# Kernel optimization log

Hardware: AMD Instinct MI355X
Metric: run time of the kernel (lower is better)

The kernel has to match this reference:

```python
import jax, jax.numpy as jnp
import numpy as np

NUM_HEADS = 16


def _window_for_epoch(epoch: int) -> int:
    # Faithful reproduction of the module's (buggy) branch structure:
    # epoch<5 sets mask_4, elif epoch<10 sets mask_6, but then an
    # independent `if epoch < 15` overwrites with mask_8, else mask_10.
    if epoch < 15:
        return 16  # mask_8 -> w=16
    return 20      # mask_10 -> w=20


def setup_inputs() -> dict:
    key = jax.random.key(0)
    ks = jax.random.split(key, 4)
    B, N, C = 2, 2048, 1024
    x = jax.random.normal(ks[0], (B, N, C), dtype=jnp.float32)
    qkv_w = jax.random.normal(ks[1], (3 * C, C), dtype=jnp.float32) * (C ** -0.5)
    proj_w = jax.random.normal(ks[2], (C, C), dtype=jnp.float32) * (C ** -0.5)
    proj_b = jnp.zeros((C,), dtype=jnp.float32)
    return {"x": x, "qkv_w": qkv_w, "proj_w": proj_w, "proj_b": proj_b, "epoch": 0}


def reference(x, qkv_w, proj_w, proj_b, epoch):
    B, N, C = x.shape
    H = NUM_HEADS
    Dh = C // H
    scale = float(Dh // H)  # head_dim // num_heads (integer division), =4

    qkv = jnp.einsum('bnc,dc->bnd', x, qkv_w)           # [B,N,3C]
    qkv = qkv.reshape(B, N, 3, H, Dh).transpose(2, 0, 3, 1, 4)
    q, k, v = qkv[0], qkv[1], qkv[2]                    # each [B,H,N,Dh]

    attn = jnp.einsum('bhnd,bhmd->bhnm', q, k) * scale  # [B,H,N,N]

    w = _window_for_epoch(int(epoch))
    idx = jnp.arange(N)
    band = jnp.abs(idx[:, None] - idx[None, :]) <= w    # [N,N] sliding window
    # Original fills masked logits with 1e-9 (NOT -inf) before softmax.
    attn = jnp.where(band[None, None], attn, jnp.float32(1e-9))
    attn = jax.nn.softmax(attn, axis=-1)

    out = jnp.einsum('bhnm,bhmd->bhnd', attn, v)        # [B,H,N,Dh]
    out = out.transpose(0, 2, 1, 3).reshape(B, N, C)
    out = jnp.einsum('bnc,dc->bnd', out, proj_w) + proj_b
    return out
```

## Files before the change

kernel.cpp:

```cpp
#include <hip/hip_runtime.h>
#include <cstddef>


typedef _Float16 f16x8 __attribute__((ext_vector_type(8)));
typedef float    f32x4 __attribute__((ext_vector_type(4)));

#define MFMA16(a, b, c) __builtin_amdgcn_mfma_f32_16x16x32_f16((a), (b), (c), 0, 0, 0)

__device__ __forceinline__ void gl_lds16(const void* g, void* l) {
    __builtin_amdgcn_global_load_lds(
        (const __attribute__((address_space(1))) void*)g,
        (__attribute__((address_space(3))) void*)l, 16, 0, 0);
}

__device__ __forceinline__ ushort f2h(float f) {
    _Float16 h = (_Float16)f;
    return *(ushort*)&h;
}

__global__ void split_all(const float* __restrict__ x,
                          const float* __restrict__ qkvw,
                          const float* __restrict__ projw,
                          ushort* __restrict__ x16,
                          ushort* __restrict__ w16,
                          ushort* __restrict__ pw16,
                          float* __restrict__ sall)
{
    const int i = blockIdx.x * 256 + threadIdx.x;
    if (i < 512) ((float4*)sall)[i] = make_float4(0.f, 0.f, 0.f, 0.f);
    const float* src; ushort* dst; int j;
    if (i < 1048576)      { src = x;     dst = x16;  j = i; }
    else if (i < 1835008) { src = qkvw;  dst = w16;  j = i - 1048576; }
    else                  { src = projw; dst = pw16; j = i - 1835008; }

    float4 v = ((const float4*)src)[j];
    ((ushort4*)dst)[j] = make_ushort4(f2h(v.x), f2h(v.y), f2h(v.z), f2h(v.w));
}

__global__ __launch_bounds__(256, 3) void gemm_mfma(
    const ushort* __restrict__ A_g, const ushort* __restrict__ W_g,
    ushort* __restrict__ out16, float* __restrict__ sall, int K)
{
    __shared__ ushort smem[16384];
    ushort* AS0 = smem;
    ushort* AS1 = smem + 4096;
    ushort* WS0 = smem + 8192;
    ushort* WS1 = smem + 12288;

    const int tid  = threadIdx.x;
    const int wid  = tid >> 6;
    const int lane = tid & 63;
    const int quad = lane >> 4;
    const int cl   = lane & 15;
    const int m0 = blockIdx.y * 128;
    const int n0 = blockIdx.x * 128;
    const int wm = (wid & 1) * 64;
    const int wn = (wid >> 1) * 64;

    const int srow = lane >> 2;
    const int scol = (lane & 3) * 8;

    const ushort* src = (wid < 2) ? A_g : W_g;
    ushort* dst = smem + wid * 4096;
    const int r0 = (wid < 2) ? m0 : n0;
    const int cofs = (wid & 1) * 32;

    f32x4 acc[4][4];
#pragma unroll
    for (int i = 0; i < 4; ++i)
#pragma unroll
        for (int j = 0; j < 4; ++j) acc[i][j] = (f32x4){0.f, 0.f, 0.f, 0.f};

    for (int k0 = 0; k0 < K; k0 += 64) {
#pragma unroll
        for (int c = 0; c < 8; ++c)
            gl_lds16(src + (size_t)(r0 + c * 16 + srow) * K + k0 + cofs + scol,
                     dst + c * 512);
        __syncthreads();

        f16x8 a0[4], w0[4];
#pragma unroll
        for (int i = 0; i < 4; ++i) {
            a0[i] = ((const f16x8*)AS0)[(wm + i * 16 + cl) * 4 + quad];
            w0[i] = ((const f16x8*)WS0)[(wn + i * 16 + cl) * 4 + quad];
        }
#pragma unroll
        for (int mi = 0; mi < 4; ++mi)
#pragma unroll
            for (int ni = 0; ni < 4; ++ni)
                acc[mi][ni] = MFMA16(a0[mi], w0[ni], acc[mi][ni]);

        f16x8 a1[4], w1[4];
#pragma unroll
        for (int i = 0; i < 4; ++i) {
            a1[i] = ((const f16x8*)AS1)[(wm + i * 16 + cl) * 4 + quad];
            w1[i] = ((const f16x8*)WS1)[(wn + i * 16 + cl) * 4 + quad];
        }
#pragma unroll
        for (int mi = 0; mi < 4; ++mi)
#pragma unroll
            for (int ni = 0; ni < 4; ++ni)
                acc[mi][ni] = MFMA16(a1[mi], w1[ni], acc[mi][ni]);
        __syncthreads();
    }

#pragma unroll
    for (int mi = 0; mi < 4; ++mi)
#pragma unroll
        for (int r = 0; r < 4; ++r) {
            const int gm = m0 + wm + mi * 16 + quad * 4 + r;
            const int b  = gm >> 11;
            const int nn = gm & 2047;
#pragma unroll
            for (int ni = 0; ni < 4; ++ni) {
                const int gn = n0 + wn + ni * 16 + cl;
                const int s  = gn >> 10;
                const int h  = (gn >> 6) & 15;
                const int dh = gn & 63;
                out16[(size_t)s * 4194304u + (((size_t)b * 16 + h) * 2048 + nn) * 64 + dh]
                    = f2h(acc[mi][ni][r]);
            }
        }

    if (n0 >= 2048) {
        const int b = (m0 + wm) >> 11;
        const int h = ((n0 + wn) >> 6) & 15;
#pragma unroll
        for (int ni = 0; ni < 4; ++ni) {
            float ps = 0.f;
#pragma unroll
            for (int mi = 0; mi < 4; ++mi)
#pragma unroll
                for (int r = 0; r < 4; ++r) ps += acc[mi][ni][r];
            ps += __shfl_xor(ps, 16);
            ps += __shfl_xor(ps, 32);
            if (quad == 0)
                atomicAdd(&sall[(b * 16 + h) * 64 + ni * 16 + cl], ps);
        }
    }
}

__global__ __launch_bounds__(256, 2) void gemm_proj(
    const ushort* __restrict__ A_g, const ushort* __restrict__ W_g,
    const float* __restrict__ bias, float* __restrict__ out)
{
    const int K = 1024, Nout = 1024;
    __shared__ ushort smem[24576];

    const int tid  = threadIdx.x;
    const int wid  = tid >> 6;
    const int lane = tid & 63;
    const int quad = lane >> 4;
    const int cl   = lane & 15;
    const int m0 = blockIdx.y * 64;
    const int n0 = blockIdx.x * 128;
    const int wm = (wid & 1) * 32;
    const int wn = (wid >> 1) * 64;

    const int srow = lane >> 2;
    const int scol = (lane & 3) * 8;

    f32x4 acc[2][4];
#pragma unroll
    for (int i = 0; i < 2; ++i)
#pragma unroll
        for (int j = 0; j < 4; ++j) acc[i][j] = (f32x4){0.f, 0.f, 0.f, 0.f};

    for (int k0 = 0; k0 < K; k0 += 128) {
#pragma unroll
        for (int c = 0; c < 12; ++c) {
            const int cid = wid * 12 + c;
            const ushort* s; ushort* d; int rr, pl;
            if (cid < 16) {
                pl = cid >> 2;
                const int ch = cid & 3;
                s = A_g; rr = m0 + ch * 16;
                d = smem + pl * 2048 + ch * 512;
            } else {
                const int wc = cid - 16;
                pl = wc >> 3;
                const int ch = wc & 7;
                s = W_g; rr = n0 + ch * 16;
                d = smem + 8192 + pl * 4096 + ch * 512;
            }
            gl_lds16(s + (size_t)(rr + srow) * K + k0 + pl * 32 + scol, d);
        }
        __syncthreads();

#pragma unroll
        for (int pl = 0; pl < 4; ++pl) {
            const ushort* ASp = smem + pl * 2048;
            const ushort* WSp = smem + 8192 + pl * 4096;
            f16x8 a[2], w[4];
#pragma unroll
            for (int i = 0; i < 2; ++i)
                a[i] = ((const f16x8*)ASp)[(wm + i * 16 + cl) * 4 + quad];
#pragma unroll
            for (int i = 0; i < 4; ++i)
                w[i] = ((const f16x8*)WSp)[(wn + i * 16 + cl) * 4 + quad];
#pragma unroll
            for (int mi = 0; mi < 2; ++mi)
#pragma unroll
                for (int ni = 0; ni < 4; ++ni)
                    acc[mi][ni] = MFMA16(a[mi], w[ni], acc[mi][ni]);
        }
        __syncthreads();
    }

    float bb[4];
#pragma unroll
    for (int ni = 0; ni < 4; ++ni) bb[ni] = bias[n0 + wn + ni * 16 + cl];
#pragma unroll
    for (int mi = 0; mi < 2; ++mi)
#pragma unroll
        for (int r = 0; r < 4; ++r) {
            const int gm = m0 + wm + mi * 16 + quad * 4 + r;
            float* rowp = out + (size_t)gm * Nout;
#pragma unroll
            for (int ni = 0; ni < 4; ++ni) {
                const int gn = n0 + wn + ni * 16 + cl;
                rowp[gn] = acc[mi][ni][r] + bb[ni];
            }
        }
}

__global__ __launch_bounds__(512) void attn_mfma(
    const ushort* __restrict__ qg, const ushort* __restrict__ kg,
    const ushort* __restrict__ vg,
    const float* __restrict__ sall,
    ushort* __restrict__ outp,
    const int* __restrict__ epoch_ptr)
{
    const int N = 2048;
    const int w = (epoch_ptr[0] < 15) ? 16 : 20;

    __shared__ ushort Pl[8][16][72];
    __shared__ ushort VT[64][180];

    const int tid  = threadIdx.x;
    const int wid  = tid >> 6;
    const int lane = tid & 63;
    const int quad = lane >> 4;
    const int cl   = lane & 15;

    const int bh = blockIdx.x >> 4;
    const int n0 = (blockIdx.x & 15) << 7;
    const int lo = max(0, n0 - w);
    const int wm = wid << 4;
    const int hi = min(N - 1, n0 + 127 + w);
    const int cnt = hi - lo + 1;

    for (int t = tid; t < 64 * 26; t += 512) {
        const int row = t / 26;
        const int c2  = 128 + (t - row * 26) * 2;
        *(unsigned*)&VT[row][c2] = 0u;
    }
    __syncthreads();

    for (int t = tid; t < 168 * 8; t += 512) {
        const int s  = t >> 3;
        const int db = (t & 7) * 8;
        if (s < cnt) {
            uint4 vv = *(const uint4*)(vg + (((size_t)bh * N) + lo + s) * 64 + db);
            VT[db + 0][s] = (ushort)(vv.x & 0xffff); VT[db + 1][s] = (ushort)(vv.x >> 16);
            VT[db + 2][s] = (ushort)(vv.y & 0xffff); VT[db + 3][s] = (ushort)(vv.y >> 16);
            VT[db + 4][s] = (ushort)(vv.z & 0xffff); VT[db + 5][s] = (ushort)(vv.z >> 16);
            VT[db + 6][s] = (ushort)(vv.w & 0xffff); VT[db + 7][s] = (ushort)(vv.w >> 16);
        }
    }

    const int jminw = max(0, n0 + wm - w);
    const int sbase = ((jminw - lo) >> 3) << 3;

    const ushort* qp = qg + ((size_t)bh * N + n0 + wm + cl) * 64;
    const f16x8 aq0 = *(const f16x8*)(qp + quad * 8);
    const f16x8 aq1 = *(const f16x8*)(qp + 32 + quad * 8);

    f32x4 sacc[4];
#pragma unroll
    for (int ni = 0; ni < 4; ++ni) {
        int krow = lo + sbase + ni * 16 + cl;
        krow = min(krow, N - 1);
        const ushort* kp = kg + ((size_t)bh * N + krow) * 64;
        const f16x8 bk0 = *(const f16x8*)(kp + quad * 8);
        const f16x8 bk1 = *(const f16x8*)(kp + 32 + quad * 8);
        f32x4 s = (f32x4){0.f, 0.f, 0.f, 0.f};
        s = MFMA16(aq0, bk0, s);
        s = MFMA16(aq1, bk1, s);
        sacc[ni] = s;
    }
#pragma unroll
    for (int ni = 0; ni < 4; ++ni) sacc[ni] *= 4.0f;

    float pm[4];
#pragma unroll
    for (int r = 0; r < 4; ++r) {
        const int n = n0 + wm + quad * 4 + r;
        const int jlo = max(0, n - w), jhi = min(N - 1, n + w);
        const int bc = jhi - jlo + 1;
        float mx = 1e-9f;
#pragma unroll
        for (int ni = 0; ni < 4; ++ni) {
            const int j = lo + sbase + ni * 16 + cl;
            const bool val = (j >= n - w) && (j <= n + w) && (j < N);
            const float sv = sacc[ni][r];
            if (val) mx = fmaxf(mx, sv);
        }
        mx = fmaxf(mx, __shfl_xor(mx, 1));
        mx = fmaxf(mx, __shfl_xor(mx, 2));
        mx = fmaxf(mx, __shfl_xor(mx, 4));
        mx = fmaxf(mx, __shfl_xor(mx, 8));
        const float em = __expf(1e-9f - mx);
        float e[4];
        float sum = 0.f;
#pragma unroll
        for (int ni = 0; ni < 4; ++ni) {
            const int j = lo + sbase + ni * 16 + cl;
            const bool val = (j >= n - w) && (j <= n + w) && (j < N);
            const float ev = val ? __expf(sacc[ni][r] - mx) : 0.f;
            e[ni] = val ? (ev - em) : 0.f;
            sum += ev;
        }
        sum += __shfl_xor(sum, 1);
        sum += __shfl_xor(sum, 2);
        sum += __shfl_xor(sum, 4);
        sum += __shfl_xor(sum, 8);
        const float inv = __builtin_amdgcn_rcpf((float)(N - bc) * em + sum);
        pm[r] = em * inv;
#pragma unroll
        for (int ni = 0; ni < 4; ++ni)
            sacc[ni][r] = e[ni] * inv;
    }

#pragma unroll
    for (int ni = 0; ni < 4; ++ni)
#pragma unroll
        for (int r = 0; r < 4; ++r)
            Pl[wid][quad * 4 + r][ni * 16 + cl] = f2h(sacc[ni][r]);

    __syncthreads();

    const int b = bh >> 4, h = bh & 15;
#pragma unroll
    for (int dn = 0; dn < 4; ++dn) {
        f32x4 o = (f32x4){0.f, 0.f, 0.f, 0.f};
#pragma unroll
        for (int k0 = 0; k0 < 64; k0 += 32) {
            const f16x8 a  = *(const f16x8*)&Pl[wid][cl][k0 + quad * 8];
            const f16x8 bb = *(const f16x8*)&VT[dn * 16 + cl][sbase + k0 + quad * 8];
            o = MFMA16(a, bb, o);
        }
        const int d = dn * 16 + cl;
        const float sv = sall[bh * 64 + d];
#pragma unroll
        for (int r = 0; r < 4; ++r) {
            const int n = n0 + wm + quad * 4 + r;
            outp[((size_t)b * N + n) * 1024 + h * 64 + d] = f2h(o[r] + pm[r] * sv);
        }
    }
}

extern "C" void kernel_launch(void* const* d_in, const int* in_sizes, int n_in,
                              void* d_out, int out_size, void* d_ws, size_t ws_size,
                              hipStream_t stream)
{
    const float* x      = (const float*)d_in[0];
    const float* qkv_w  = (const float*)d_in[1];
    const float* proj_w = (const float*)d_in[2];
    const float* proj_b = (const float*)d_in[3];
    const int*   epoch  = (const int*)d_in[4];
    float* out = (float*)d_out;

    const size_t BHND = (size_t)2 * 16 * 2048 * 64;
    const size_t XN = 4194304, WN = 3145728;

    ushort* qkv16 = (ushort*)d_ws;
    ushort* q16   = qkv16;
    ushort* k16   = qkv16 + BHND;
    ushort* v16   = qkv16 + 2 * BHND;
    float*  sall  = (float*)(qkv16 + 3 * BHND);
    ushort* x16   = (ushort*)(sall + 4096);
    ushort* w16   = x16 + XN;
    ushort* pw16  = w16 + WN;
    ushort* ao    = x16;

    split_all<<<dim3(8192), dim3(256), 0, stream>>>(
        x, qkv_w, proj_w, x16, w16, pw16, sall);

    gemm_mfma<<<dim3(24, 32), dim3(256), 0, stream>>>(x16, w16, qkv16, sall, 1024);

    attn_mfma<<<dim3(512), dim3(512), 0, stream>>>(q16, k16, v16, sall, ao, epoch);

    gemm_proj<<<dim3(8, 64), dim3(256), 0, stream>>>(ao, pw16, proj_b, out);
}
```

Before: 148.1 us.

## Rewrite QKV GEMM with 5-stage async LDS pipeline and larger swizzled tiles

Replaces the QKV projection GEMM with a 512-thread kernel using 256x192 tiles, a five-buffer global-to-LDS prefetch ring with partial vmcnt waits, XOR-swizzled LDS layout, block-index remapping for L2 locality, and raised MFMA priority. It is meant to hide global load latency behind MFMA work, cut LDS bank conflicts and improve data reuse compared with the single-stage 128x128 kernel that synchronised twice per K step. The trade-off is heavy LDS use (about 144 KB per block) and a 96-register accumulator per thread, which lowers occupancy, plus a grid of exactly 256 blocks.

New measurement: 145.3 us. About the same (-1.9%).

```diff
diff --git a/kernel.cpp b/kernel.cpp
--- a/kernel.cpp
+++ b/kernel.cpp
@@ -37,105 +37,148 @@
     ((ushort4*)dst)[j] = make_ushort4(f2h(v.x), f2h(v.y), f2h(v.z), f2h(v.w));
 }
 
-__global__ __launch_bounds__(256, 3) void gemm_mfma(
+__global__ __launch_bounds__(512, 2) void gemm_qkv_pipe(
     const ushort* __restrict__ A_g, const ushort* __restrict__ W_g,
-    ushort* __restrict__ out16, float* __restrict__ sall, int K)
+    ushort* __restrict__ out16, float* __restrict__ sall)
 {
-    __shared__ ushort smem[16384];
-    ushort* AS0 = smem;
-    ushort* AS1 = smem + 4096;
-    ushort* WS0 = smem + 8192;
-    ushort* WS1 = smem + 12288;
+    const int K = 1024;
+    __shared__ ushort sm[73728];
 
     const int tid  = threadIdx.x;
     const int wid  = tid >> 6;
     const int lane = tid & 63;
     const int quad = lane >> 4;
     const int cl   = lane & 15;
-    const int m0 = blockIdx.y * 128;
-    const int n0 = blockIdx.x * 128;
-    const int wm = (wid & 1) * 64;
-    const int wn = (wid >> 1) * 64;
-
-    const int srow = lane >> 2;
-    const int scol = (lane & 3) * 8;
-
-    const ushort* src = (wid < 2) ? A_g : W_g;
-    ushort* dst = smem + wid * 4096;
-    const int r0 = (wid < 2) ? m0 : n0;
-    const int cofs = (wid & 1) * 32;
-
-    f32x4 acc[4][4];
-#pragma unroll
-    for (int i = 0; i < 4; ++i)
-#pragma unroll
-        for (int j = 0; j < 4; ++j) acc[i][j] = (f32x4){0.f, 0.f, 0.f, 0.f};
-
-    for (int k0 = 0; k0 < K; k0 += 64) {
-#pragma unroll
-        for (int c = 0; c < 8; ++c)
-            gl_lds16(src + (size_t)(r0 + c * 16 + srow) * K + k0 + cofs + scol,
-                     dst + c * 512);
-        __syncthreads();
-
-        f16x8 a0[4], w0[4];
-#pragma unroll
-        for (int i = 0; i < 4; ++i) {
-            a0[i] = ((const f16x8*)AS0)[(wm + i * 16 + cl) * 4 + quad];
-            w0[i] = ((const f16x8*)WS0)[(wn + i * 16 + cl) * 4 + quad];
-        }
-#pragma unroll
-        for (int mi = 0; mi < 4; ++mi)
-#pragma unroll
-            for (int ni = 0; ni < 4; ++ni)
-                acc[mi][ni] = MFMA16(a0[mi], w0[ni], acc[mi][ni]);
-
-        f16x8 a1[4], w1[4];
-#pragma unroll
-        for (int i = 0; i < 4; ++i) {
-            a1[i] = ((const f16x8*)AS1)[(wm + i * 16 + cl) * 4 + quad];
-            w1[i] = ((const f16x8*)WS1)[(wn + i * 16 + cl) * 4 + quad];
-        }
-#pragma unroll
-        for (int mi = 0; mi < 4; ++mi)
-#pragma unroll
-            for (int ni = 0; ni < 4; ++ni)
-                acc[mi][ni] = MFMA16(a1[mi], w1[ni], acc[mi][ni]);
-        __syncthreads();
-    }
-
-#pragma unroll
-    for (int mi = 0; mi < 4; ++mi)
+
+    const int bsw = (blockIdx.x & 7) * 32 + (blockIdx.x >> 3);
+    const int m0 = (bsw >> 4) * 256;
+    const int n0 = (bsw & 15) * 192;
+
+    const int wr = wid >> 2;
+    const int wc = wid & 3;
+
+    const int lrow = lane >> 2;
+    const int sl   = lane & 3;
+    const int rA1 = wid * 16 + lrow;
+    const int rA2 = 128 + rA1;
+    const int rB1 = wid * 16 + lrow;
+    const int rB2 = 128 + (wid & 3) * 16 + lrow;
+
+    const ushort* sA1 = A_g + (size_t)(m0 + rA1) * K + ((sl ^ ((rA1 >> 1) & 3)) * 8);
+    const ushort* sA2 = A_g + (size_t)(m0 + rA2) * K + ((sl ^ ((rA2 >> 1) & 3)) * 8);
+    const ushort* sB1 = W_g + (size_t)(n0 + rB1) * K + ((sl ^ ((rB1 >> 1) & 3)) * 8);
+    const ushort* sB2 = W_g + (size_t)(n0 + rB2) * K + ((sl ^ ((rB2 >> 1) & 3)) * 8);
+
+    const int dA1 = wid * 512;
+    const int dA2 = 4096 + wid * 512;
+    const int dB1 = 8192 + wid * 512;
+
+    int aoff[8], boff[3];
+#pragma unroll
+    for (int mg = 0; mg < 8; ++mg) {
+        const int row = wr * 128 + mg * 16 + cl;
+        aoff[mg] = row * 32 + ((quad ^ ((row >> 1) & 3)) * 8);
+    }
+#pragma unroll
+    for (int ng = 0; ng < 3; ++ng) {
+        const int row = wc * 48 + ng * 16 + cl;
+        boff[ng] = 8192 + row * 32 + ((quad ^ ((row >> 1) & 3)) * 8);
+    }
+
+    f32x4 acc[8][3];
+#pragma unroll
+    for (int mg = 0; mg < 8; ++mg)
+#pragma unroll
+        for (int ng = 0; ng < 3; ++ng) acc[mg][ng] = (f32x4){0.f, 0.f, 0.f, 0.f};
+
+    int kst = 0;
+
+#define STAGE_T(BUF) do {                                                    \
+    const int bo_ = (BUF) * 14336;                                           \
+    gl_lds16(sA1 + kst, sm + bo_ + dA1);                                     \
+    gl_lds16(sA2 + kst, sm + bo_ + dA2);                                     \
+    gl_lds16(sB1 + kst, sm + bo_ + dB1);                                     \
+    ushort* pB2_ = (wid < 4) ? (sm + bo_ + 12288 + wid * 512)                \
+                             : (sm + 71680 + (wid & 3) * 512);               \
+    gl_lds16(sB2 + kst, pB2_);                                               \
+    kst += 32;                                                               \
+} while (0)
+
+#define COMPUTE_T(BUF) do {                                                  \
+    const int co_ = (BUF) * 14336;                                           \
+    f16x8 af[8]; f16x8 bf[3];                                                \
+    _Pragma("unroll")                                                        \
+    for (int mg = 0; mg < 8; ++mg) af[mg] = *(const f16x8*)&sm[co_ + aoff[mg]]; \
+    _Pragma("unroll")                                                        \
+    for (int ng = 0; ng < 3; ++ng) bf[ng] = *(const f16x8*)&sm[co_ + boff[ng]]; \
+    __builtin_amdgcn_s_setprio(1);                                           \
+    _Pragma("unroll")                                                        \
+    for (int mg = 0; mg < 8; ++mg)                                           \
+        _Pragma("unroll")                                                    \
+        for (int ng = 0; ng < 3; ++ng)                                       \
+            acc[mg][ng] = MFMA16(af[mg], bf[ng], acc[mg][ng]);               \
+    __builtin_amdgcn_s_setprio(0);                                           \
+} while (0)
+
+#define WAITBAR(N) do {                                                      \
+    asm volatile("s_waitcnt vmcnt(" #N ")" ::: "memory");                    \
+    __builtin_amdgcn_s_barrier();                                            \
+    asm volatile("" ::: "memory");                                           \
+} while (0)
+
+    STAGE_T(0); STAGE_T(1); STAGE_T(2); STAGE_T(3);
+
+    int bc = 0, bs = 4;
+    for (int t = 0; t < 28; ++t) {
+        WAITBAR(12);
+        STAGE_T(bs);
+        COMPUTE_T(bc);
+        bc = (bc == 4) ? 0 : bc + 1;
+        bs = (bs == 4) ? 0 : bs + 1;
+    }
+    WAITBAR(12); COMPUTE_T(bc); bc = (bc == 4) ? 0 : bc + 1;
+    WAITBAR(8);  COMPUTE_T(bc); bc = (bc == 4) ? 0 : bc + 1;
+    WAITBAR(4);  COMPUTE_T(bc); bc = (bc == 4) ? 0 : bc + 1;
+    WAITBAR(0);  COMPUTE_T(bc);
+
+#undef STAGE_T
+#undef COMPUTE_T
+#undef WAITBAR
+
+#pragma unroll
+    for (int mg = 0; mg < 8; ++mg)
 #pragma unroll
         for (int r = 0; r < 4; ++r) {
-            const int gm = m0 + wm + mi * 16 + quad * 4 + r;
-            const int b  = gm >> 11;
+            const int gm = m0 + wr * 128 + mg * 16 + quad * 4 + r;
+            const int bq = gm >> 11;
             const int nn = gm & 2047;
 #pragma unroll
-            for (int ni = 0; ni < 4; ++ni) {
-                const int gn = n0 + wn + ni * 16 + cl;
-                const int s  = gn >> 10;
+            for (int ng = 0; ng < 3; ++ng) {
+                const int gn = n0 + wc * 48 + ng * 16 + cl;
+                const int sq = gn >> 10;
                 const int h  = (gn >> 6) & 15;
                 const int dh = gn & 63;
-                out16[(size_t)s * 4194304u + (((size_t)b * 16 + h) * 2048 + nn) * 64 + dh]
-                    = f2h(acc[mi][ni][r]);
+                out16[(size_t)sq * 4194304u + (((size_t)bq * 16 + h) * 2048 + nn) * 64 + dh]
+                    = f2h(acc[mg][ng][r]);
             }
         }
 
-    if (n0 >= 2048) {
-        const int b = (m0 + wm) >> 11;
-        const int h = ((n0 + wn) >> 6) & 15;
-#pragma unroll
-        for (int ni = 0; ni < 4; ++ni) {
+    const int bq2 = (m0 + wr * 128) >> 11;
+#pragma unroll
+    for (int ng = 0; ng < 3; ++ng) {
+        const int gbase = n0 + wc * 48 + ng * 16;
+        if (gbase >= 2048) {
             float ps = 0.f;
 #pragma unroll
-            for (int mi = 0; mi < 4; ++mi)
-#pragma unroll
-                for (int r = 0; r < 4; ++r) ps += acc[mi][ni][r];
+            for (int mg = 0; mg < 8; ++mg)
+#pragma unroll
+                for (int r = 0; r < 4; ++r) ps += acc[mg][ng][r];
             ps += __shfl_xor(ps, 16);
             ps += __shfl_xor(ps, 32);
-            if (quad == 0)
-                atomicAdd(&sall[(b * 16 + h) * 64 + ni * 16 + cl], ps);
+            if (quad == 0) {
+                const int h = (gbase >> 6) & 15;
+                atomicAdd(&sall[(bq2 * 16 + h) * 64 + (gbase & 63) + cl], ps);
+            }
         }
     }
 }
@@ -177,9 +220,9 @@
                 s = A_g; rr = m0 + ch * 16;
                 d = smem + pl * 2048 + ch * 512;
             } else {
-                const int wc = cid - 16;
-                pl = wc >> 3;
-                const int ch = wc & 7;
+                const int wcx = cid - 16;
+                pl = wcx >> 3;
+                const int ch = wcx & 7;
                 s = W_g; rr = n0 + ch * 16;
                 d = smem + 8192 + pl * 4096 + ch * 512;
             }
@@ -387,7 +430,7 @@
     split_all<<<dim3(8192), dim3(256), 0, stream>>>(
         x, qkv_w, proj_w, x16, w16, pw16, sall);
 
-    gemm_mfma<<<dim3(24, 32), dim3(256), 0, stream>>>(x16, w16, qkv16, sall, 1024);
+    gemm_qkv_pipe<<<dim3(256), dim3(512), 0, stream>>>(x16, w16, qkv16, sall);
 
     attn_mfma<<<dim3(512), dim3(512), 0, stream>>>(q16, k16, v16, sall, ao, epoch);
 
```
